# Kernel optimization log

Measured on AMD Instinct MI355X. Metric: run time of the kernel, lower is better.

Reference implementation:

```python
import jax, jax.numpy as jnp
import numpy as np


def setup_inputs() -> dict:
    key = jax.random.key(0)
    H, W, N = 4096, 4096, 8
    label = jax.random.randint(key, (H, W), 0, N, dtype=jnp.int64 if jax.config.read('jax_enable_x64') else jnp.int32).astype(jnp.int32)
    return {"label": label, "N": N}


def reference(label, N):
    # torch: eye(N).index_select(0, label.view(-1)).view(H, W, N).permute(2, 0, 1)
    # == one_hot over last axis, then move class axis to front -> (N, H, W)
    oh = jax.nn.one_hot(label, N, dtype=jnp.float32)  # (H, W, N)
    return jnp.transpose(oh, (2, 0, 1))  # (N, H, W)
```

## Files before the change

### kernel.cpp

```cpp
#include <hip/hip_runtime.h>
#include <hip/hip_bf16.h>


typedef unsigned int u32;

#define PITER 16
#define CHUNK_PX (PITER * 1024)

__global__ void __launch_bounds__(256) get_one_hot_59442347376951_kernel(
    const int* __restrict__ label, float* __restrict__ out, int total) {
    const int tid = threadIdx.x;
    const long long base = (long long)blockIdx.x * CHUNK_PX;

    u32 pk[PITER];
#pragma unroll
    for (int it = 0; it < PITER; ++it) {
        int4 a = *reinterpret_cast<const int4*>(label + base + it * 1024 + tid * 4);
        pk[it] = (u32)(a.x & 255) | ((u32)(a.y & 255) << 8) |
                 ((u32)(a.z & 255) << 16) | ((u32)(a.w & 255) << 24);
    }

    for (u32 n = 0; n < 8; ++n) {
        float* op = out + (long long)n * total + base;
#pragma unroll
        for (int it = 0; it < PITER; ++it) {
            u32 w = pk[it];
            float4 v;
            v.x = (((w      ) & 255u) == n) ? 1.0f : 0.0f;
            v.y = (((w >> 8 ) & 255u) == n) ? 1.0f : 0.0f;
            v.z = (((w >> 16) & 255u) == n) ? 1.0f : 0.0f;
            v.w = (((w >> 24)       ) == n) ? 1.0f : 0.0f;
            *reinterpret_cast<float4*>(op + it * 1024 + tid * 4) = v;
        }
    }
}

__global__ void __launch_bounds__(256) get_one_hot_generic_kernel(
    const int* __restrict__ label, float* __restrict__ out,
    int total, int N) {
    long long i = ((long long)blockIdx.x * blockDim.x + threadIdx.x) * 4;
    if (i >= total) return;
    int4 lab = *reinterpret_cast<const int4*>(label + i);
    for (int n = 0; n < N; ++n) {
        float4 v;
        v.x = (lab.x == n) ? 1.0f : 0.0f;
        v.y = (lab.y == n) ? 1.0f : 0.0f;
        v.z = (lab.z == n) ? 1.0f : 0.0f;
        v.w = (lab.w == n) ? 1.0f : 0.0f;
        *reinterpret_cast<float4*>(out + (long long)n * total + i) = v;
    }
}

extern "C" void kernel_launch(void* const* d_in, const int* in_sizes, int n_in,
                              void* d_out, int out_size, void* d_ws, size_t ws_size,
                              hipStream_t stream) {
    const int* label = (const int*)d_in[0];
    float* out = (float*)d_out;

    int total = in_sizes[0];
    int N = out_size / total;

    if (N == 8 && total % CHUNK_PX == 0) {
        int grid = total / CHUNK_PX;
        get_one_hot_59442347376951_kernel<<<grid, 256, 0, stream>>>(label, out, total);
    } else {
        int grid = (total / 4 + 255) / 256;
        get_one_hot_generic_kernel<<<grid, 256, 0, stream>>>(label, out, total, N);
    }
}
```

Measured before the change: 129.2 us.

## Split one-hot into label packing pass and per-class expand kernel

Labels are first packed into bytes in a workspace buffer by a separate kernel. A second kernel then launches a 2D grid with one block row per class, expanding the packed labels to float outputs. This raises the block count and parallelism of the write-dominated expansion. In exchange it adds an extra launch, a workspace round trip, and eight re-reads of the packed buffer, and it needs workspace of sufficient size.

New measurement: 120.4 us. 6.9% less time.

```diff
diff --git a/kernel.cpp b/kernel.cpp
--- a/kernel.cpp
+++ b/kernel.cpp
@@ -4,34 +4,35 @@
 
 typedef unsigned int u32;
 
-#define PITER 16
-#define CHUNK_PX (PITER * 1024)
+__global__ void __launch_bounds__(256) pack_labels_kernel(
+    const int* __restrict__ label, u32* __restrict__ packed) {
+    const int tid = threadIdx.x;
+    const long long base = (long long)blockIdx.x * 4096;
+    u32* pp = packed + (base >> 2);
+#pragma unroll
+    for (int it = 0; it < 4; ++it) {
+        int4 a = *reinterpret_cast<const int4*>(label + base + it * 1024 + tid * 4);
+        pp[it * 256 + tid] = (u32)(a.x & 255) | ((u32)(a.y & 255) << 8) |
+                             ((u32)(a.z & 255) << 16) | ((u32)(a.w & 255) << 24);
+    }
+}
 
-__global__ void __launch_bounds__(256) get_one_hot_59442347376951_kernel(
-    const int* __restrict__ label, float* __restrict__ out, int total) {
+__global__ void __launch_bounds__(256) expand_kernel(
+    const u32* __restrict__ packed, float* __restrict__ out, int total) {
+    const u32 n = blockIdx.y;
     const int tid = threadIdx.x;
-    const long long base = (long long)blockIdx.x * CHUNK_PX;
-
-    u32 pk[PITER];
+    const long long base = (long long)blockIdx.x * 4096;
+    const u32* pp = packed + (base >> 2);
+    float* op = out + (long long)n * total + base;
 #pragma unroll
-    for (int it = 0; it < PITER; ++it) {
-        int4 a = *reinterpret_cast<const int4*>(label + base + it * 1024 + tid * 4);
-        pk[it] = (u32)(a.x & 255) | ((u32)(a.y & 255) << 8) |
-                 ((u32)(a.z & 255) << 16) | ((u32)(a.w & 255) << 24);
-    }
-
-    for (u32 n = 0; n < 8; ++n) {
-        float* op = out + (long long)n * total + base;
-#pragma unroll
-        for (int it = 0; it < PITER; ++it) {
-            u32 w = pk[it];
-            float4 v;
-            v.x = (((w      ) & 255u) == n) ? 1.0f : 0.0f;
-            v.y = (((w >> 8 ) & 255u) == n) ? 1.0f : 0.0f;
-            v.z = (((w >> 16) & 255u) == n) ? 1.0f : 0.0f;
-            v.w = (((w >> 24)       ) == n) ? 1.0f : 0.0f;
-            *reinterpret_cast<float4*>(op + it * 1024 + tid * 4) = v;
-        }
+    for (int it = 0; it < 4; ++it) {
+        u32 w = pp[it * 256 + tid];
+        float4 v;
+        v.x = (((w      ) & 255u) == n) ? 1.0f : 0.0f;
+        v.y = (((w >> 8 ) & 255u) == n) ? 1.0f : 0.0f;
+        v.z = (((w >> 16) & 255u) == n) ? 1.0f : 0.0f;
+        v.w = (((w >> 24)       ) == n) ? 1.0f : 0.0f;
+        *reinterpret_cast<float4*>(op + it * 1024 + tid * 4) = v;
     }
 }
 
@@ -60,9 +61,12 @@
     int total = in_sizes[0];
     int N = out_size / total;
 
-    if (N == 8 && total % CHUNK_PX == 0) {
-        int grid = total / CHUNK_PX;
-        get_one_hot_59442347376951_kernel<<<grid, 256, 0, stream>>>(label, out, total);
+    bool fast = (N == 8) && (total % 4096 == 0) && (ws_size >= (size_t)total);
+    if (fast) {
+        int blocks = total / 4096;
+        pack_labels_kernel<<<blocks, 256, 0, stream>>>(label, (u32*)d_ws);
+        dim3 grid(blocks, N);
+        expand_kernel<<<grid, 256, 0, stream>>>((const u32*)d_ws, out, total);
     } else {
         int grid = (total / 4 + 255) / 256;
         get_one_hot_generic_kernel<<<grid, 256, 0, stream>>>(label, out, total, N);
```
